# Kernel tuning notes

Measured on AMD Instinct MI355X. Metric: run time of the kernel, lower is better.

## Reference

```python
import jax, jax.numpy as jnp
import numpy as np
from jax import lax

BN_EPS = 1e-5

def conv1d(x, w, b):
    # x: [B,C,L], w: [O,I,K], padding 'same' for k=3
    y = lax.conv_general_dilated(x, w, window_strides=(1,), padding=[(1, 1)],
                                 dimension_numbers=("NCH", "OIH", "NCH"))
    return y + b[None, :, None]

def bn_eval(x, g, b, m, v):
    return (x - m[None, :, None]) / jnp.sqrt(v[None, :, None] + BN_EPS) * g[None, :, None] + b[None, :, None]

def maxpool2(x):
    B, C, L = x.shape
    return x.reshape(B, C, L // 2, 2).max(axis=-1)

def expert_block(x, w, b, g, be, m, v):
    return maxpool2(jax.nn.relu(bn_eval(conv1d(x, w, b), g, be, m, v)))

def setup_inputs() -> dict:
    key = jax.random.key(0)
    ks = jax.random.split(key, 40)
    B, L, E, C = 1024, 2048, 4, 5
    d = {"x": jax.random.normal(ks[0], (B, 1, L), jnp.float32)}
    d["conv1_w"] = jax.random.normal(ks[1], (8, 1, 3), jnp.float32) * 0.2
    d["conv1_b"] = jax.random.normal(ks[2], (8,), jnp.float32) * 0.02
    # stacked expert params, leading dim = num_experts
    chans = [(16, 8), (32, 16), (64, 32)]
    i = 3
    for blk, (co, ci) in enumerate(chans, start=1):
        d[f"ew{blk}"] = jax.random.normal(ks[i], (E, co, ci, 3), jnp.float32) * (1.0 / np.sqrt(ci * 3)); i += 1
        d[f"eb{blk}"] = jax.random.normal(ks[i], (E, co), jnp.float32) * 0.02; i += 1
        d[f"ebn{blk}_g"] = 0.5 + jax.random.uniform(ks[i], (E, co), jnp.float32); i += 1
        d[f"ebn{blk}_b"] = jax.random.normal(ks[i], (E, co), jnp.float32) * 0.02; i += 1
        d[f"ebn{blk}_m"] = jax.random.normal(ks[i], (E, co), jnp.float32) * 0.1; i += 1
        d[f"ebn{blk}_v"] = 0.5 + jax.random.uniform(ks[i], (E, co), jnp.float32); i += 1
    d["router_w"] = jax.random.normal(ks[i], (E, 8), jnp.float32) * 0.3; i += 1
    d["router_b"] = jnp.zeros((E,), jnp.float32)
    final_length = L // 8 * 64
    d["fc1_w"] = jax.random.normal(ks[i], (64, final_length), jnp.float32) * 0.01; i += 1
    d["fc1_b"] = jnp.zeros((64,), jnp.float32)
    d["fc2_w"] = jax.random.normal(ks[i], (C, 64), jnp.float32) * 0.1; i += 1
    d["fc2_b"] = jnp.zeros((C,), jnp.float32)
    return d

TOP_K = 2

def reference(x, conv1_w, conv1_b,
              ew1, eb1, ebn1_g, ebn1_b, ebn1_m, ebn1_v,
              ew2, eb2, ebn2_g, ebn2_b, ebn2_m, ebn2_v,
              ew3, eb3, ebn3_g, ebn3_b, ebn3_m, ebn3_v,
              router_w, router_b, fc1_w, fc1_b, fc2_w, fc2_b):
    B = x.shape[0]
    E = router_w.shape[0]
    h = jax.nn.relu(conv1d(x, conv1_w, conv1_b))           # [B,8,L]
    pooled = h.mean(axis=-1)                               # [B,8] (AdaptiveAvgPool1d(1))
    logits = pooled @ router_w.T + router_b                # [B,E]
    probs = jax.nn.softmax(logits, axis=-1)
    topk_gates, topk_idx = lax.top_k(probs, TOP_K)         # [B,K]
    topk_gates = topk_gates / topk_gates.sum(axis=-1, keepdims=True)
    # dense gate matrix [B,E]: zero where expert not in top-k
    onehot = jax.nn.one_hot(topk_idx, E, dtype=h.dtype)    # [B,K,E]
    gate = (topk_gates[..., None] * onehot).sum(axis=1)    # [B,E]
    # run every expert on the full batch (mathematically identical combine)
    def run_expert(p):
        w1, b1, g1, be1, m1, v1, w2, b2, g2, be2, m2, v2, w3, b3, g3, be3, m3, v3 = p
        o = expert_block(h, w1, b1, g1, be1, m1, v1)
        o = expert_block(o, w2, b2, g2, be2, m2, v2)
        o = expert_block(o, w3, b3, g3, be3, m3, v3)
        return o                                           # [B,64,L//8]
    eparams = (ew1, eb1, ebn1_g, ebn1_b, ebn1_m, ebn1_v,
               ew2, eb2, ebn2_g, ebn2_b, ebn2_m, ebn2_v,
               ew3, eb3, ebn3_g, ebn3_b, ebn3_m, ebn3_v)
    expert_outs = jax.vmap(run_expert)(eparams)            # [E,B,64,L//8]
    combined = jnp.einsum("ebcl,be->bcl", expert_outs, gate)
    flat = combined.reshape(B, -1)
    z = jax.nn.relu(flat @ fc1_w.T + fc1_b)                # dropout inactive in eval
    out = z @ fc2_w.T + fc2_b
    mean_probs = probs.mean(axis=0)
    cv = jnp.std(mean_probs, ddof=1) / (mean_probs.mean() + 1e-10)
    aux_loss = cv ** 2
    return out, aux_loss
```

## Files before the change

kernel.cpp:

```cpp
#include <hip/hip_runtime.h>

constexpr int L0 = 2048;
constexpr size_t OFF_POOLED = 0;
constexpr size_t OFF_TOPKI  = 8192;
constexpr size_t OFF_TOPKG  = 10240;
constexpr size_t OFF_B1     = 12288;
constexpr size_t OFF_B2     = 12352;
constexpr size_t OFF_B3     = 12480;
constexpr size_t OFF_W1Q    = 12800;
constexpr size_t OFF_W2Q    = 14848;
constexpr size_t OFF_W3Q    = 23040;
constexpr size_t OFF_COMB   = 57344;
constexpr size_t OFF_P      = 57344 + 16777216;

__global__ __launch_bounds__(256) void pool_kernel(const float* __restrict__ x,
    const float* __restrict__ c1w, const float* __restrict__ c1b, float* __restrict__ pooled)
{
    __shared__ float xbuf[2050];
    __shared__ float part[4][8];
    int b = blockIdx.x, tid = threadIdx.x;
    const float* xr = x + (size_t)b * L0;
    for (int i = tid; i < 2050; i += 256) xbuf[i] = (i >= 1 && i <= L0) ? xr[i - 1] : 0.f;
    __syncthreads();
    float w[24], bb[8];
#pragma unroll
    for (int i = 0; i < 24; i++) w[i] = c1w[i];
#pragma unroll
    for (int c = 0; c < 8; c++) bb[c] = c1b[c];
    float acc[8];
#pragma unroll
    for (int c = 0; c < 8; c++) acc[c] = 0.f;
    for (int l = tid; l < L0; l += 256) {
        float xm = xbuf[l], x0 = xbuf[l + 1], xp = xbuf[l + 2];
#pragma unroll
        for (int c = 0; c < 8; c++)
            acc[c] += fmaxf(fmaf(w[3 * c], xm, fmaf(w[3 * c + 1], x0, fmaf(w[3 * c + 2], xp, bb[c]))), 0.f);
    }
#pragma unroll
    for (int c = 0; c < 8; c++) {
#pragma unroll
        for (int off = 32; off > 0; off >>= 1)
            acc[c] += __shfl_down(acc[c], off, 64);
    }
    int wv = tid >> 6, ln = tid & 63;
    if (ln == 0) {
#pragma unroll
        for (int c = 0; c < 8; c++) part[wv][c] = acc[c];
    }
    __syncthreads();
    if (tid < 8) {
        float s = part[0][tid] + part[1][tid] + part[2][tid] + part[3][tid];
        pooled[b * 8 + tid] = s * (1.f / L0);
    }
}

__global__ __launch_bounds__(256) void repack_kernel(
    const float* __restrict__ ew1, const float* __restrict__ eb1, const float* __restrict__ g1,
    const float* __restrict__ bb1, const float* __restrict__ m1, const float* __restrict__ v1,
    const float* __restrict__ ew2, const float* __restrict__ eb2, const float* __restrict__ g2,
    const float* __restrict__ bb2, const float* __restrict__ m2, const float* __restrict__ v2,
    const float* __restrict__ ew3, const float* __restrict__ eb3, const float* __restrict__ g3,
    const float* __restrict__ bb3, const float* __restrict__ m3, const float* __restrict__ v3,
    float* __restrict__ w1q, float* __restrict__ w2q, float* __restrict__ w3q,
    float* __restrict__ b1p, float* __restrict__ b2p, float* __restrict__ b3p)
{
    int i = blockIdx.x * 256 + threadIdx.x;
    if (i < 2048) {
        int k = i & 3, ci = (i >> 2) & 7, co = (i >> 5) & 15, e = i >> 9;
        int ec = e * 16 + co;
        float A = g1[ec] * rsqrtf(v1[ec] + 1e-5f);
        w1q[i] = (k < 3) ? ew1[(ec * 8 + ci) * 3 + k] * A : 0.f;
    } else if (i < 10240) {
        int ii = i - 2048;
        int k = ii & 3, ci = (ii >> 2) & 15, co = (ii >> 6) & 31, e = ii >> 11;
        int ec = e * 32 + co;
        float A = g2[ec] * rsqrtf(v2[ec] + 1e-5f);
        w2q[ii] = (k < 3) ? ew2[(ec * 16 + ci) * 3 + k] * A : 0.f;
    } else if (i < 43008) {
        int ii = i - 10240;
        int k = ii & 3, ci = (ii >> 2) & 31, co = (ii >> 7) & 63, e = ii >> 13;
        int ec = e * 64 + co;
        float A = g3[ec] * rsqrtf(v3[ec] + 1e-5f);
        w3q[ii] = (k < 3) ? ew3[(ec * 32 + ci) * 3 + k] * A : 0.f;
    } else if (i < 43456) {
        int j = i - 43008;
        if (j < 64)       { float A = g1[j] * rsqrtf(v1[j] + 1e-5f); b1p[j] = fmaf(eb1[j] - m1[j], A, bb1[j]); }
        else if (j < 192) { int q = j - 64;  float A = g2[q] * rsqrtf(v2[q] + 1e-5f); b2p[q] = fmaf(eb2[q] - m2[q], A, bb2[q]); }
        else              { int q = j - 192; float A = g3[q] * rsqrtf(v3[q] + 1e-5f); b3p[q] = fmaf(eb3[q] - m3[q], A, bb3[q]); }
    }
}

__global__ __launch_bounds__(1024) void router_kernel(const float* __restrict__ pooled,
    const float* __restrict__ rw, const float* __restrict__ rb,
    int* __restrict__ tidx, float* __restrict__ tg, float* __restrict__ aux)
{
    __shared__ float pr[4][1024];
    int b = threadIdx.x;
    float p[8];
#pragma unroll
    for (int c = 0; c < 8; c++) p[c] = pooled[b * 8 + c];
    float lg[4];
#pragma unroll
    for (int e = 0; e < 4; e++) {
        float a = rb[e];
#pragma unroll
        for (int c = 0; c < 8; c++) a = fmaf(p[c], rw[e * 8 + c], a);
        lg[e] = a;
    }
    float m = fmaxf(fmaxf(lg[0], lg[1]), fmaxf(lg[2], lg[3]));
    float pe[4]; float s = 0.f;
#pragma unroll
    for (int e = 0; e < 4; e++) { pe[e] = expf(lg[e] - m); s += pe[e]; }
    float inv = 1.f / s;
#pragma unroll
    for (int e = 0; e < 4; e++) pe[e] *= inv;
    int e0 = 0;
#pragma unroll
    for (int e = 1; e < 4; e++) if (pe[e] > pe[e0]) e0 = e;
    int e1 = -1;
#pragma unroll
    for (int e = 0; e < 4; e++) if (e != e0 && (e1 < 0 || pe[e] > pe[e1])) e1 = e;
    float s2 = pe[e0] + pe[e1];
    tidx[b * 2] = e0; tidx[b * 2 + 1] = e1;
    tg[b * 2] = pe[e0] / s2; tg[b * 2 + 1] = pe[e1] / s2;
#pragma unroll
    for (int e = 0; e < 4; e++) pr[e][b] = pe[e];
    __syncthreads();
    for (int off = 512; off > 0; off >>= 1) {
        if (b < off) {
#pragma unroll
            for (int e = 0; e < 4; e++) pr[e][b] += pr[e][b + off];
        }
        __syncthreads();
    }
    if (b == 0) {
        float mp[4]; float mm = 0.f;
#pragma unroll
        for (int e = 0; e < 4; e++) { mp[e] = pr[e][0] * (1.f / 1024.f); mm += mp[e]; }
        mm *= 0.25f;
        float var = 0.f;
#pragma unroll
        for (int e = 0; e < 4; e++) { float d = mp[e] - mm; var += d * d; }
        var *= (1.f / 3.f);
        float cv = sqrtf(var) / (mm + 1e-10f);
        aux[0] = cv * cv;
    }
}

constexpr int XB_OFF = 0;
constexpr int E0_OFF = 288;
constexpr int O0_OFF = 1472;
constexpr int E1_OFF = 2656;
constexpr int O1_OFF = 3872;
constexpr int E2_OFF = 5088;
constexpr int O2_OFF = 6240;
constexpr int LDS_FLOATS = 7392;

template<int CI, int SIN>
__device__ __forceinline__ void conv1ch8(
    const float* __restrict__ wq,
    const float bias,
    const float* __restrict__ Ein, const float* __restrict__ Oin,
    const int j0, float vE[8], float vO[8])
{
#pragma unroll
    for (int p = 0; p < 8; ++p) { vE[p] = bias; vO[p] = bias; }
#pragma unroll
    for (int ci = 0; ci < CI; ++ci) {
        const float4 w = *reinterpret_cast<const float4*>(wq + ci * 4);
        const float* ep = Ein + ci * SIN + j0;
        const float4 ea = *reinterpret_cast<const float4*>(ep);
        const float4 eb = *reinterpret_cast<const float4*>(ep + 4);
        const float e8 = ep[8];
        const float* op = Oin + ci * SIN + j0;
        const float4 oa = *reinterpret_cast<const float4*>(op);
        const float4 ob = *reinterpret_cast<const float4*>(op + 4);
        const float o8 = op[8];
        const float E[9] = {ea.x, ea.y, ea.z, ea.w, eb.x, eb.y, eb.z, eb.w, e8};
        const float O[9] = {oa.x, oa.y, oa.z, oa.w, ob.x, ob.y, ob.z, ob.w, o8};
#pragma unroll
        for (int p = 0; p < 8; ++p) {
            vE[p] = fmaf(w.x, E[p], fmaf(w.y, O[p], fmaf(w.z, E[p + 1], vE[p])));
            vO[p] = fmaf(w.x, O[p], fmaf(w.y, E[p + 1], fmaf(w.z, O[p + 1], vO[p])));
        }
    }
}

template<int SOUT, int LOUT, bool GUARDJ>
__device__ __forceinline__ void pool_store(
    const float vE[8], const float vO[8],
    float* __restrict__ Eout, float* __restrict__ Oout,
    const int co, const int j0, const int a_out, const int jmax)
{
    float v[8];
#pragma unroll
    for (int p = 0; p < 8; ++p) {
        int l = a_out + j0 + p;
        bool ok = (l >= 0) && (l < LOUT);
        if (GUARDJ) ok = ok && (j0 + p < jmax);
        v[p] = ok ? fmaxf(fmaxf(vE[p], vO[p]), 0.f) : 0.f;
    }
    *reinterpret_cast<float4*>(Eout + co * SOUT + (j0 >> 1)) = make_float4(v[0], v[2], v[4], v[6]);
    *reinterpret_cast<float4*>(Oout + co * SOUT + (j0 >> 1)) = make_float4(v[1], v[3], v[5], v[7]);
}

__global__ __launch_bounds__(256, 5) void expert_kernel(
    const float* __restrict__ x, const float* __restrict__ c1w, const float* __restrict__ c1b,
    const float* __restrict__ w1q, const float* __restrict__ w2q, const float* __restrict__ w3q,
    const float* __restrict__ b1p, const float* __restrict__ b2p, const float* __restrict__ b3p,
    const int* __restrict__ tidx, const float* __restrict__ tg,
    float* __restrict__ comb)
{
    __shared__ __align__(16) float lds[LDS_FLOATS];
    const int tid = threadIdx.x;
    const int bt = blockIdx.x;
    const int b = bt >> 3, t = bt & 7;
    const int a3 = t * 32, a2 = 2 * a3 - 1, a1 = 4 * a3 - 3, a0 = 8 * a3 - 7;
    const float* xr = x + (size_t)b * L0;
    float* xb = lds + XB_OFF;
    for (int m = tid; m < 284; m += 256) {
        int gpos = a0 - 1 + m;
        xb[m] = (gpos >= 0 && gpos < L0) ? xr[gpos] : 0.f;
    }
    __syncthreads();
    {
        const int ch = tid & 7;
        const int pj = tid >> 3;
        float wa = c1w[ch * 3], wb = c1w[ch * 3 + 1], wc = c1w[ch * 3 + 2], bc = c1b[ch];
        float* tgt = lds + ((pj & 1) ? O0_OFF : E0_OFF) + ch * 148;
        const int kb = pj >> 1;
        for (int k = 0; k < 9; ++k) {
            int j = pj + 32 * k;
            if (j >= 282) break;
            int l = a0 + j;
            float v = 0.f;
            if (l >= 0 && l < L0)
                v = fmaxf(fmaf(wa, xb[j], fmaf(wb, xb[j + 1], fmaf(wc, xb[j + 2], bc))), 0.f);
            tgt[kb + 16 * k] = v;
        }
    }
    const int ea = tidx[b * 2], eb2i = tidx[b * 2 + 1];
    const float ga = tg[b * 2], gb2 = tg[b * 2 + 1];
    const int co1 = tid & 15, pg1 = tid >> 4;
    const int co2 = tid & 31, pg2 = tid >> 5;
    const int co3 = tid >> 2, pg3 = tid & 3;
    const int j3 = 8 * pg3;
    float oacc[8];
#pragma unroll
    for (int p = 0; p < 8; p++) oacc[p] = 0.f;
    float vE[8], vO[8];
#pragma unroll 1
    for (int slot = 0; slot < 2; ++slot) {
        const int e = slot ? eb2i : ea;
        const float g = slot ? gb2 : ga;
        __syncthreads();
        {
            const float* wq = w1q + (size_t)(e * 16 + co1) * 32;
            const float bias = b1p[e * 16 + co1];
            conv1ch8<8, 148>(wq, bias, lds + E0_OFF, lds + O0_OFF, 8 * pg1, vE, vO);
            pool_store<76, 1024, false>(vE, vO, lds + E1_OFF, lds + O1_OFF, co1, 8 * pg1, a1, 138);
            if (pg1 < 2) {
                int j0 = 128 + 8 * pg1;
                conv1ch8<8, 148>(wq, bias, lds + E0_OFF, lds + O0_OFF, j0, vE, vO);
                pool_store<76, 1024, true>(vE, vO, lds + E1_OFF, lds + O1_OFF, co1, j0, a1, 138);
            }
        }
        __syncthreads();
        {
            const float* wq = w2q + (size_t)(e * 32 + co2) * 64;
            const float bias = b2p[e * 32 + co2];
            conv1ch8<16, 76>(wq, bias, lds + E1_OFF, lds + O1_OFF, 8 * pg2, vE, vO);
            pool_store<36, 512, false>(vE, vO, lds + E2_OFF, lds + O2_OFF, co2, 8 * pg2, a2, 66);
            if (pg2 == 0) {
                conv1ch8<16, 76>(wq, bias, lds + E1_OFF, lds + O1_OFF, 64, vE, vO);
                pool_store<36, 512, true>(vE, vO, lds + E2_OFF, lds + O2_OFF, co2, 64, a2, 66);
            }
        }
        __syncthreads();
        {
            const float* wq = w3q + (size_t)(e * 64 + co3) * 128;
            const float bias = b3p[e * 64 + co3];
            conv1ch8<32, 36>(wq, bias, lds + E2_OFF, lds + O2_OFF, j3, vE, vO);
#pragma unroll
            for (int p = 0; p < 8; ++p)
                oacc[p] = fmaf(g, fmaxf(fmaxf(vE[p], vO[p]), 0.f), oacc[p]);
        }
    }
    float* cb = comb + (size_t)b * 16384 + (size_t)co3 * 256 + a3 + j3;
    *reinterpret_cast<float4*>(cb)     = make_float4(oacc[0], oacc[1], oacc[2], oacc[3]);
    *reinterpret_cast<float4*>(cb + 4) = make_float4(oacc[4], oacc[5], oacc[6], oacc[7]);
}

__global__ __launch_bounds__(256) void fc1_kernel(const float* __restrict__ comb,
    const float* __restrict__ w, float* __restrict__ P)
{
    __shared__ __align__(16) float at[64 * 65];
    __shared__ __align__(16) float wt[64 * 65];
    int bc = blockIdx.x;
    int kc = blockIdx.y;
    int tid = threadIdx.x;
    int tx = tid & 15, ty = tid >> 4;
    float acc[4][4];
#pragma unroll
    for (int i = 0; i < 4; i++)
#pragma unroll
        for (int j = 0; j < 4; j++) acc[i][j] = 0.f;
    int b0 = bc * 64;
    for (int kt = 0; kt < 16; ++kt) {
        int k0 = kc * 1024 + kt * 64;
        __syncthreads();
        for (int i = tid; i < 4096; i += 256) {
            int r = i >> 6, kk = i & 63;
            at[r * 65 + kk] = comb[(size_t)(b0 + r) * 16384 + k0 + kk];
            wt[r * 65 + kk] = w[(size_t)r * 16384 + k0 + kk];
        }
        __syncthreads();
#pragma unroll 8
        for (int kk = 0; kk < 64; kk++) {
            float av[4], wv[4];
#pragma unroll
            for (int i = 0; i < 4; i++) av[i] = at[(ty * 4 + i) * 65 + kk];
#pragma unroll
            for (int j = 0; j < 4; j++) wv[j] = wt[(tx * 4 + j) * 65 + kk];
#pragma unroll
            for (int i = 0; i < 4; i++)
#pragma unroll
                for (int j = 0; j < 4; j++) acc[i][j] = fmaf(av[i], wv[j], acc[i][j]);
        }
    }
    float* Pp = P + (size_t)kc * 65536;
#pragma unroll
    for (int i = 0; i < 4; i++)
#pragma unroll
        for (int j = 0; j < 4; j++)
            Pp[(size_t)(b0 + ty * 4 + i) * 64 + tx * 4 + j] = acc[i][j];
}

__global__ __launch_bounds__(64) void fc2_kernel(const float* __restrict__ P,
    const float* __restrict__ f1b, const float* __restrict__ w2, const float* __restrict__ b2,
    float* __restrict__ out)
{
    int b = blockIdx.x * 64 + threadIdx.x;
    float z[64];
#pragma unroll
    for (int n = 0; n < 64; n++) z[n] = 0.f;
    for (int kc = 0; kc < 16; kc++) {
        const float* Pp = P + (size_t)kc * 65536 + (size_t)b * 64;
#pragma unroll
        for (int n = 0; n < 64; n++) z[n] += Pp[n];
    }
    float o[5] = {0.f, 0.f, 0.f, 0.f, 0.f};
#pragma unroll
    for (int n = 0; n < 64; n++) {
        float zz = fmaxf(z[n] + f1b[n], 0.f);
#pragma unroll
        for (int c = 0; c < 5; c++) o[c] = fmaf(zz, w2[c * 64 + n], o[c]);
    }
#pragma unroll
    for (int c = 0; c < 5; c++) out[b * 5 + c] = o[c] + b2[c];
}

extern "C" void kernel_launch(void* const* d_in, const int* in_sizes, int n_in,
                              void* d_out, int out_size, void* d_ws, size_t ws_size,
                              hipStream_t stream)
{
    const float* x   = (const float*)d_in[0];
    const float* c1w = (const float*)d_in[1];
    const float* c1b = (const float*)d_in[2];
    const float* ew1 = (const float*)d_in[3];
    const float* eb1 = (const float*)d_in[4];
    const float* g1  = (const float*)d_in[5];
    const float* bb1 = (const float*)d_in[6];
    const float* m1  = (const float*)d_in[7];
    const float* v1  = (const float*)d_in[8];
    const float* ew2 = (const float*)d_in[9];
    const float* eb2 = (const float*)d_in[10];
    const float* g2  = (const float*)d_in[11];
    const float* bb2 = (const float*)d_in[12];
    const float* m2  = (const float*)d_in[13];
    const float* v2  = (const float*)d_in[14];
    const float* ew3 = (const float*)d_in[15];
    const float* eb3 = (const float*)d_in[16];
    const float* g3  = (const float*)d_in[17];
    const float* bb3 = (const float*)d_in[18];
    const float* m3  = (const float*)d_in[19];
    const float* v3  = (const float*)d_in[20];
    const float* rw  = (const float*)d_in[21];
    const float* rb  = (const float*)d_in[22];
    const float* f1w = (const float*)d_in[23];
    const float* f1b = (const float*)d_in[24];
    const float* f2w = (const float*)d_in[25];
    const float* f2b = (const float*)d_in[26];

    float* ws     = (float*)d_ws;
    float* pooled = ws + OFF_POOLED;
    int*   tidx   = (int*)(ws + OFF_TOPKI);
    float* tg     = ws + OFF_TOPKG;
    float* b1p    = ws + OFF_B1;
    float* b2p    = ws + OFF_B2;
    float* b3p    = ws + OFF_B3;
    float* w1q    = ws + OFF_W1Q;
    float* w2q    = ws + OFF_W2Q;
    float* w3q    = ws + OFF_W3Q;
    float* comb   = ws + OFF_COMB;
    float* P      = ws + OFF_P;
    float* out    = (float*)d_out;

    hipLaunchKernelGGL(pool_kernel, dim3(1024), dim3(256), 0, stream, x, c1w, c1b, pooled);
    hipLaunchKernelGGL(repack_kernel, dim3(170), dim3(256), 0, stream,
                       ew1, eb1, g1, bb1, m1, v1, ew2, eb2, g2, bb2, m2, v2,
                       ew3, eb3, g3, bb3, m3, v3, w1q, w2q, w3q, b1p, b2p, b3p);
    hipLaunchKernelGGL(router_kernel, dim3(1), dim3(1024), 0, stream, pooled, rw, rb, tidx, tg, out + 5120);
    hipLaunchKernelGGL(expert_kernel, dim3(8192), dim3(256), 0, stream,
                       x, c1w, c1b, w1q, w2q, w3q, b1p, b2p, b3p, tidx, tg, comb);
    hipLaunchKernelGGL(fc1_kernel, dim3(16, 16), dim3(256), 0, stream, comb, f1w, P);
    hipLaunchKernelGGL(fc2_kernel, dim3(16), dim3(64), 0, stream, P, f1b, f2w, f2b, out);
}
```

Baseline: 409.8 us.

## Run both top-k experts concurrently per block with two output channels per thread

```diff
diff --git a/kernel.cpp b/kernel.cpp
--- a/kernel.cpp
+++ b/kernel.cpp
@@ -66,20 +66,20 @@
 {
     int i = blockIdx.x * 256 + threadIdx.x;
     if (i < 2048) {
-        int k = i & 3, ci = (i >> 2) & 7, co = (i >> 5) & 15, e = i >> 9;
-        int ec = e * 16 + co;
+        int k = i & 3, c = (i >> 2) & 1, ci = (i >> 3) & 7, cp = (i >> 6) & 7, e = i >> 9;
+        int ec = e * 16 + 2 * cp + c;
         float A = g1[ec] * rsqrtf(v1[ec] + 1e-5f);
         w1q[i] = (k < 3) ? ew1[(ec * 8 + ci) * 3 + k] * A : 0.f;
     } else if (i < 10240) {
         int ii = i - 2048;
-        int k = ii & 3, ci = (ii >> 2) & 15, co = (ii >> 6) & 31, e = ii >> 11;
-        int ec = e * 32 + co;
+        int k = ii & 3, c = (ii >> 2) & 1, ci = (ii >> 3) & 15, cp = (ii >> 7) & 15, e = ii >> 11;
+        int ec = e * 32 + 2 * cp + c;
         float A = g2[ec] * rsqrtf(v2[ec] + 1e-5f);
         w2q[ii] = (k < 3) ? ew2[(ec * 16 + ci) * 3 + k] * A : 0.f;
     } else if (i < 43008) {
         int ii = i - 10240;
-        int k = ii & 3, ci = (ii >> 2) & 31, co = (ii >> 7) & 63, e = ii >> 13;
-        int ec = e * 64 + co;
+        int k = ii & 3, c = (ii >> 2) & 1, ci = (ii >> 3) & 31, cp = (ii >> 8) & 31, e = ii >> 13;
+        int ec = e * 64 + 2 * cp + c;
         float A = g3[ec] * rsqrtf(v3[ec] + 1e-5f);
         w3q[ii] = (k < 3) ? ew3[(ec * 32 + ci) * 3 + k] * A : 0.f;
     } else if (i < 43456) {
@@ -147,64 +147,71 @@
     }
 }
 
-constexpr int XB_OFF = 0;
-constexpr int E0_OFF = 288;
-constexpr int O0_OFF = 1472;
-constexpr int E1_OFF = 2656;
-constexpr int O1_OFF = 3872;
-constexpr int E2_OFF = 5088;
-constexpr int O2_OFF = 6240;
-constexpr int LDS_FLOATS = 7392;
-
-template<int CI, int SIN>
-__device__ __forceinline__ void conv1ch8(
-    const float* __restrict__ wq,
-    const float bias,
-    const float* __restrict__ Ein, const float* __restrict__ Oin,
-    const int j0, float vE[8], float vO[8])
-{
-#pragma unroll
-    for (int p = 0; p < 8; ++p) { vE[p] = bias; vO[p] = bias; }
+constexpr int XB_OFF   = 0;
+constexpr int B0_OFF   = 288;
+constexpr int S1_OFF   = 2656;
+constexpr int S2_OFF   = 7520;
+constexpr int PART_OFF = 2656;
+constexpr int LDS_FLOATS = 12128;
+
+template<int CI, int SROW>
+__device__ __forceinline__ void conv2ch8(
+    const float* __restrict__ wq, const float2 bias,
+    const float* __restrict__ in,
+    const int j0, float vE[2][8], float vO[2][8])
+{
+#pragma unroll
+    for (int p = 0; p < 8; ++p) {
+        vE[0][p] = bias.x; vO[0][p] = bias.x;
+        vE[1][p] = bias.y; vO[1][p] = bias.y;
+    }
 #pragma unroll
     for (int ci = 0; ci < CI; ++ci) {
-        const float4 w = *reinterpret_cast<const float4*>(wq + ci * 4);
-        const float* ep = Ein + ci * SIN + j0;
+        const float4 wA = *reinterpret_cast<const float4*>(wq + ci * 8);
+        const float4 wB = *reinterpret_cast<const float4*>(wq + ci * 8 + 4);
+        const float* ep = in + ci * (2 * SROW) + j0;
+        const float* op = ep + SROW;
         const float4 ea = *reinterpret_cast<const float4*>(ep);
         const float4 eb = *reinterpret_cast<const float4*>(ep + 4);
-        const float e8 = ep[8];
-        const float* op = Oin + ci * SIN + j0;
         const float4 oa = *reinterpret_cast<const float4*>(op);
         const float4 ob = *reinterpret_cast<const float4*>(op + 4);
+        const float e8 = ep[8];
         const float o8 = op[8];
         const float E[9] = {ea.x, ea.y, ea.z, ea.w, eb.x, eb.y, eb.z, eb.w, e8};
         const float O[9] = {oa.x, oa.y, oa.z, oa.w, ob.x, ob.y, ob.z, ob.w, o8};
 #pragma unroll
         for (int p = 0; p < 8; ++p) {
-            vE[p] = fmaf(w.x, E[p], fmaf(w.y, O[p], fmaf(w.z, E[p + 1], vE[p])));
-            vO[p] = fmaf(w.x, O[p], fmaf(w.y, E[p + 1], fmaf(w.z, O[p + 1], vO[p])));
-        }
-    }
-}
-
-template<int SOUT, int LOUT, bool GUARDJ>
-__device__ __forceinline__ void pool_store(
-    const float vE[8], const float vO[8],
-    float* __restrict__ Eout, float* __restrict__ Oout,
-    const int co, const int j0, const int a_out, const int jmax)
-{
-    float v[8];
-#pragma unroll
-    for (int p = 0; p < 8; ++p) {
-        int l = a_out + j0 + p;
-        bool ok = (l >= 0) && (l < LOUT);
-        if (GUARDJ) ok = ok && (j0 + p < jmax);
-        v[p] = ok ? fmaxf(fmaxf(vE[p], vO[p]), 0.f) : 0.f;
-    }
-    *reinterpret_cast<float4*>(Eout + co * SOUT + (j0 >> 1)) = make_float4(v[0], v[2], v[4], v[6]);
-    *reinterpret_cast<float4*>(Oout + co * SOUT + (j0 >> 1)) = make_float4(v[1], v[3], v[5], v[7]);
-}
-
-__global__ __launch_bounds__(256, 5) void expert_kernel(
+            vE[0][p] = fmaf(wA.x, E[p], fmaf(wA.y, O[p], fmaf(wA.z, E[p + 1], vE[0][p])));
+            vO[0][p] = fmaf(wA.x, O[p], fmaf(wA.y, E[p + 1], fmaf(wA.z, O[p + 1], vO[0][p])));
+            vE[1][p] = fmaf(wB.x, E[p], fmaf(wB.y, O[p], fmaf(wB.z, E[p + 1], vE[1][p])));
+            vO[1][p] = fmaf(wB.x, O[p], fmaf(wB.y, E[p + 1], fmaf(wB.z, O[p + 1], vO[1][p])));
+        }
+    }
+}
+
+template<int SROW_OUT, int LOUT, bool GUARDJ>
+__device__ __forceinline__ void pool_store2(
+    const float vE[2][8], const float vO[2][8],
+    float* __restrict__ out,
+    const int co0, const int j0, const int a_out, const int jmax)
+{
+#pragma unroll
+    for (int c = 0; c < 2; ++c) {
+        float v[8];
+#pragma unroll
+        for (int p = 0; p < 8; ++p) {
+            int l = a_out + j0 + p;
+            bool ok = (l >= 0) && (l < LOUT);
+            if (GUARDJ) ok = ok && (j0 + p < jmax);
+            v[p] = ok ? fmaxf(fmaxf(vE[c][p], vO[c][p]), 0.f) : 0.f;
+        }
+        float* eo = out + (co0 + c) * (2 * SROW_OUT) + (j0 >> 1);
+        *reinterpret_cast<float4*>(eo)            = make_float4(v[0], v[2], v[4], v[6]);
+        *reinterpret_cast<float4*>(eo + SROW_OUT) = make_float4(v[1], v[3], v[5], v[7]);
+    }
+}
+
+__global__ __launch_bounds__(256, 3) void expert_kernel(
     const float* __restrict__ x, const float* __restrict__ c1w, const float* __restrict__ c1b,
     const float* __restrict__ w1q, const float* __restrict__ w2q, const float* __restrict__ w3q,
     const float* __restrict__ b1p, const float* __restrict__ b2p, const float* __restrict__ b3p,
@@ -214,20 +221,20 @@
     __shared__ __align__(16) float lds[LDS_FLOATS];
     const int tid = threadIdx.x;
     const int bt = blockIdx.x;
-    const int b = bt >> 3, t = bt & 7;
-    const int a3 = t * 32, a2 = 2 * a3 - 1, a1 = 4 * a3 - 3, a0 = 8 * a3 - 7;
+    const int b = bt >> 3, t8 = bt & 7;
+    const int a3 = t8 * 32, a2 = 2 * a3 - 1, a1 = 4 * a3 - 3, a0 = 8 * a3 - 7;
     const float* xr = x + (size_t)b * L0;
     float* xb = lds + XB_OFF;
     for (int m = tid; m < 284; m += 256) {
-        int gpos = a0 - 1 + m;
-        xb[m] = (gpos >= 0 && gpos < L0) ? xr[gpos] : 0.f;
+        int gp = a0 - 1 + m;
+        xb[m] = (gp >= 0 && gp < L0) ? xr[gp] : 0.f;
     }
     __syncthreads();
     {
         const int ch = tid & 7;
         const int pj = tid >> 3;
         float wa = c1w[ch * 3], wb = c1w[ch * 3 + 1], wc = c1w[ch * 3 + 2], bc = c1b[ch];
-        float* tgt = lds + ((pj & 1) ? O0_OFF : E0_OFF) + ch * 148;
+        float* tgt = lds + B0_OFF + ch * 296 + ((pj & 1) ? 148 : 0);
         const int kb = pj >> 1;
         for (int k = 0; k < 9; ++k) {
             int j = pj + 32 * k;
@@ -239,56 +246,71 @@
             tgt[kb + 16 * k] = v;
         }
     }
-    const int ea = tidx[b * 2], eb2i = tidx[b * 2 + 1];
-    const float ga = tg[b * 2], gb2 = tg[b * 2 + 1];
-    const int co1 = tid & 15, pg1 = tid >> 4;
-    const int co2 = tid & 31, pg2 = tid >> 5;
-    const int co3 = tid >> 2, pg3 = tid & 3;
-    const int j3 = 8 * pg3;
-    float oacc[8];
-#pragma unroll
-    for (int p = 0; p < 8; p++) oacc[p] = 0.f;
-    float vE[8], vO[8];
-#pragma unroll 1
-    for (int slot = 0; slot < 2; ++slot) {
-        const int e = slot ? eb2i : ea;
-        const float g = slot ? gb2 : ga;
-        __syncthreads();
-        {
-            const float* wq = w1q + (size_t)(e * 16 + co1) * 32;
-            const float bias = b1p[e * 16 + co1];
-            conv1ch8<8, 148>(wq, bias, lds + E0_OFF, lds + O0_OFF, 8 * pg1, vE, vO);
-            pool_store<76, 1024, false>(vE, vO, lds + E1_OFF, lds + O1_OFF, co1, 8 * pg1, a1, 138);
-            if (pg1 < 2) {
-                int j0 = 128 + 8 * pg1;
-                conv1ch8<8, 148>(wq, bias, lds + E0_OFF, lds + O0_OFF, j0, vE, vO);
-                pool_store<76, 1024, true>(vE, vO, lds + E1_OFF, lds + O1_OFF, co1, j0, a1, 138);
-            }
-        }
-        __syncthreads();
-        {
-            const float* wq = w2q + (size_t)(e * 32 + co2) * 64;
-            const float bias = b2p[e * 32 + co2];
-            conv1ch8<16, 76>(wq, bias, lds + E1_OFF, lds + O1_OFF, 8 * pg2, vE, vO);
-            pool_store<36, 512, false>(vE, vO, lds + E2_OFF, lds + O2_OFF, co2, 8 * pg2, a2, 66);
-            if (pg2 == 0) {
-                conv1ch8<16, 76>(wq, bias, lds + E1_OFF, lds + O1_OFF, 64, vE, vO);
-                pool_store<36, 512, true>(vE, vO, lds + E2_OFF, lds + O2_OFF, co2, 64, a2, 66);
-            }
-        }
-        __syncthreads();
-        {
-            const float* wq = w3q + (size_t)(e * 64 + co3) * 128;
-            const float bias = b3p[e * 64 + co3];
-            conv1ch8<32, 36>(wq, bias, lds + E2_OFF, lds + O2_OFF, j3, vE, vO);
+    const int half = tid >> 7;
+    const int t = tid & 127;
+    const int e = tidx[b * 2 + half];
+    const float g = tg[b * 2 + half];
+    float* S1 = lds + S1_OFF + half * 2432;
+    float* S2 = lds + S2_OFF + half * 2304;
+    float vE[2][8], vO[2][8];
+    __syncthreads();
+    {
+        const int cg = t & 7, pg = t >> 3;
+        const float* wq = w1q + (size_t)(e * 8 + cg) * 64;
+        const float2 bb = *reinterpret_cast<const float2*>(b1p + e * 16 + 2 * cg);
+        conv2ch8<8, 148>(wq, bb, lds + B0_OFF, 8 * pg, vE, vO);
+        pool_store2<76, 1024, false>(vE, vO, S1, 2 * cg, 8 * pg, a1, 138);
+        if (pg < 2) {
+            const int j0 = 128 + 8 * pg;
+            conv2ch8<8, 148>(wq, bb, lds + B0_OFF, j0, vE, vO);
+            pool_store2<76, 1024, true>(vE, vO, S1, 2 * cg, j0, a1, 138);
+        }
+    }
+    __syncthreads();
+    {
+        const int cg = t & 15, pg = t >> 4;
+        const float* wq = w2q + (size_t)(e * 16 + cg) * 128;
+        const float2 bb = *reinterpret_cast<const float2*>(b2p + e * 32 + 2 * cg);
+        conv2ch8<16, 76>(wq, bb, S1, 8 * pg, vE, vO);
+        pool_store2<36, 512, false>(vE, vO, S2, 2 * cg, 8 * pg, a2, 66);
+        if (pg == 0) {
+            conv2ch8<16, 76>(wq, bb, S1, 64, vE, vO);
+            pool_store2<36, 512, true>(vE, vO, S2, 2 * cg, 64, a2, 66);
+        }
+    }
+    __syncthreads();
+    {
+        const int cg = t >> 2, pg = t & 3;
+        const int j3 = 8 * pg;
+        const float* wq = w3q + (size_t)(e * 32 + cg) * 256;
+        const float2 bb = *reinterpret_cast<const float2*>(b3p + e * 64 + 2 * cg);
+        conv2ch8<32, 36>(wq, bb, S2, j3, vE, vO);
+        float* pp = lds + PART_OFF + half * 2304 + (2 * cg) * 36 + j3;
+#pragma unroll
+        for (int c = 0; c < 2; ++c) {
+            float v[8];
 #pragma unroll
             for (int p = 0; p < 8; ++p)
-                oacc[p] = fmaf(g, fmaxf(fmaxf(vE[p], vO[p]), 0.f), oacc[p]);
-        }
-    }
-    float* cb = comb + (size_t)b * 16384 + (size_t)co3 * 256 + a3 + j3;
-    *reinterpret_cast<float4*>(cb)     = make_float4(oacc[0], oacc[1], oacc[2], oacc[3]);
-    *reinterpret_cast<float4*>(cb + 4) = make_float4(oacc[4], oacc[5], oacc[6], oacc[7]);
+                v[p] = g * fmaxf(fmaxf(vE[c][p], vO[c][p]), 0.f);
+            *reinterpret_cast<float4*>(pp + c * 36)     = make_float4(v[0], v[1], v[2], v[3]);
+            *reinterpret_cast<float4*>(pp + c * 36 + 4) = make_float4(v[4], v[5], v[6], v[7]);
+        }
+    }
+    __syncthreads();
+    {
+        const float* P0 = lds + PART_OFF;
+        const float* P1 = P0 + 2304;
+        float* cb = comb + (size_t)b * 16384 + a3;
+#pragma unroll
+        for (int r0 = 0; r0 < 2; ++r0) {
+            int r = tid + 256 * r0;
+            int co = r >> 3, j = (r & 7) * 4;
+            float4 u0 = *reinterpret_cast<const float4*>(P0 + co * 36 + j);
+            float4 u1 = *reinterpret_cast<const float4*>(P1 + co * 36 + j);
+            *reinterpret_cast<float4*>(cb + (size_t)co * 256 + j) =
+                make_float4(u0.x + u1.x, u0.y + u1.y, u0.z + u1.z, u0.w + u1.w);
+        }
+    }
 }
 
 __global__ __launch_bounds__(256) void fc1_kernel(const float* __restrict__ comb,
```

Result: slower. 1.349 ms (+229.1%).
